# Kernel optimization log

Hardware: AMD Instinct MI355X
Metric: run time of the kernel (lower is better)

The kernel has to match this reference:

```python
import jax, jax.numpy as jnp
import numpy as np
from jax import lax

B, T = 64, 200
NUM_C, DIM_S, SIZE_M = 2000, 128, 50


def setup_inputs() -> dict:
    key = jax.random.key(0)
    ks = jax.random.split(key, 12)
    d = {}
    d['skill'] = jax.random.randint(ks[0], (B, T), 0, NUM_C)
    d['answer'] = jax.random.randint(ks[1], (B, T), 0, 2)
    s = 1.0 / np.sqrt(DIM_S)
    d['k_emb'] = jax.random.normal(ks[2], (NUM_C + 1, DIM_S), jnp.float32)
    d['v_emb'] = jax.random.normal(ks[3], (2 * NUM_C + 1, DIM_S), jnp.float32)
    # kaiming_normal on [size_m, dim_s]: std = sqrt(2/dim_s)
    d['Mk'] = jax.random.normal(ks[4], (SIZE_M, DIM_S), jnp.float32) * np.sqrt(2.0 / DIM_S)
    d['Mv0'] = jax.random.normal(ks[5], (SIZE_M, DIM_S), jnp.float32) * np.sqrt(2.0 / DIM_S)
    d['f_W'] = jax.random.normal(ks[6], (DIM_S, 2 * DIM_S), jnp.float32) * (1.0 / np.sqrt(2 * DIM_S))
    d['f_b'] = jnp.zeros((DIM_S,), jnp.float32)
    d['p_W'] = jax.random.normal(ks[7], (NUM_C, DIM_S), jnp.float32) * s
    d['p_b'] = jnp.zeros((NUM_C,), jnp.float32)
    d['e_W'] = jax.random.normal(ks[8], (DIM_S, DIM_S), jnp.float32) * s
    d['e_b'] = jnp.zeros((DIM_S,), jnp.float32)
    d['a_W'] = jax.random.normal(ks[9], (DIM_S, DIM_S), jnp.float32) * s
    d['a_b'] = jnp.zeros((DIM_S,), jnp.float32)
    return d


def reference(skill, answer, k_emb, v_emb, Mk, Mv0, f_W, f_b, p_W, p_b, e_W, e_b, a_W, a_b):
    num_c = p_W.shape[0]
    bsz = skill.shape[0]
    answer_x = jnp.where(answer == 2, 1, answer)
    x = skill + num_c * answer_x                       # [B,T]
    k = k_emb[skill]                                   # [B,T,D]
    v = v_emb[x]                                       # [B,T,D]
    w = jax.nn.softmax(jnp.einsum('btd,md->btm', k, Mk), axis=-1)   # [B,T,M]
    e = jax.nn.sigmoid(jnp.einsum('btd,ed->bte', v, e_W) + e_b)      # [B,T,D]
    a = jnp.tanh(jnp.einsum('btd,ed->bte', v, a_W) + a_b)            # [B,T,D]

    Mv_init = jnp.broadcast_to(Mv0, (bsz,) + Mv0.shape)              # [B,M,D]

    def step(Mvt, inp):
        et, at, wt = inp                               # [B,D],[B,D],[B,M]
        # read uses pre-update memory (Mv[:, :-1] in the torch code)
        read = jnp.einsum('bm,bmd->bd', wt, Mvt)
        Mvt_new = Mvt * (1.0 - wt[:, :, None] * et[:, None, :]) + wt[:, :, None] * at[:, None, :]
        return Mvt_new, read

    _, reads = lax.scan(step, Mv_init,
                        (e.transpose(1, 0, 2), a.transpose(1, 0, 2), w.transpose(1, 0, 2)))
    reads = reads.transpose(1, 0, 2)                   # [B,T,D]

    f = jnp.tanh(jnp.concatenate([reads, k], axis=-1) @ f_W.T + f_b)  # [B,T,D]
    p = jax.nn.sigmoid(f @ p_W.T + p_b)                # [B,T,num_c] (dropout is identity at eval)
    p = p[:, :-1, :]
    next_skill = skill[:, 1:]                          # [B,T-1]
    idx = jnp.minimum(next_skill, num_c - 1)
    pred = jnp.take_along_axis(p, idx[..., None], axis=-1)[..., 0]
    pred = jnp.where(next_skill < num_c, pred, 0.0)    # index num_c -> zero row in torch one_hot
    return pred
```

## Files before the change

kernel.cpp:

```cpp
#include <hip/hip_runtime.h>
#include <math.h>

#define Bsz 64
#define Tn 200
#define NUMC 2000
#define DS 128
#define SM 50
#define NTOK (Bsz*Tn)
#define WG2 10
#define MPG2 5

typedef __attribute__((ext_vector_type(8))) short bfrag;
typedef __attribute__((ext_vector_type(4))) float f32x4;
typedef __attribute__((ext_vector_type(4))) unsigned int u32x4;

__device__ __forceinline__ unsigned short f2bf(float x) {
    unsigned int u = __builtin_bit_cast(unsigned int, x);
    u = u + 0x7fffu + ((u >> 16) & 1u);
    return (unsigned short)(u >> 16);
}
__device__ __forceinline__ unsigned int pack2(float a, float b) {
    return (unsigned int)f2bf(a) | ((unsigned int)f2bf(b) << 16);
}
__device__ __forceinline__ bfrag mk_frag(f32x4 x, f32x4 y) {
    u32x4 t;
    t[0] = pack2(x[0], x[1]); t[1] = pack2(x[2], x[3]);
    t[2] = pack2(y[0], y[1]); t[3] = pack2(y[2], y[3]);
    return __builtin_bit_cast(bfrag, t);
}

__device__ __forceinline__ float fast_exp(float x)  { return __builtin_amdgcn_exp2f(x * 1.44269504f); }
__device__ __forceinline__ float fast_rcp(float x)  { return __builtin_amdgcn_rcpf(x); }
__device__ __forceinline__ float fast_sigmoid(float x) { return fast_rcp(1.f + fast_exp(-x)); }
__device__ __forceinline__ float fast_tanh(float x) { return 1.f - 2.f * fast_rcp(fast_exp(2.f * x) + 1.f); }

__device__ __forceinline__ void load_group(const bfrag* __restrict__ B, int nt0, int L, bfrag bf[4][4]) {
    #pragma unroll
    for (int t = 0; t < 4; t++)
        #pragma unroll
        for (int ki = 0; ki < 4; ki++)
            bf[t][ki] = B[(size_t)((nt0 + t) * 4 + ki) * 64 + L];
}
__device__ __forceinline__ void mfma_group(const bfrag A[4], const bfrag bf[4][4], f32x4 acc[4]) {
    #pragma unroll
    for (int ki = 0; ki < 4; ki++)
        #pragma unroll
        for (int t = 0; t < 4; t++)
            acc[t] = __builtin_amdgcn_mfma_f32_16x16x32_bf16(A[ki], bf[t][ki], acc[t], 0, 0, 0);
}

__global__ __launch_bounds__(256) void k0_cast(
    const float* __restrict__ eW, const float* __restrict__ aW,
    const float* __restrict__ fW, const float* __restrict__ Mk,
    unsigned int* __restrict__ BeaU, unsigned int* __restrict__ BkmU,
    unsigned int* __restrict__ Bf0U)
{
    const int g = blockIdx.x * 256 + threadIdx.x;
    if (g >= 9216) return;
    int gm, mat;
    unsigned int* dst;
    if (g < 4096)      { mat = 0; gm = g;        dst = BeaU; }
    else if (g < 7168) { mat = 1; gm = g - 4096; dst = BkmU; }
    else               { mat = 2; gm = g - 7168; dst = Bf0U; }
    const int nt = gm >> 8, r = gm & 255, ki = r >> 6, L = r & 63;
    const int n = nt * 16 + (L & 15);
    const int k = ki * 32 + (L >> 4) * 8;

    const float* src = nullptr;
    if (mat == 0) {
        src = (n < 128) ? (eW + (size_t)n * DS + k) : (aW + (size_t)(n - 128) * DS + k);
    } else if (mat == 1) {
        if (n < 128)      src = fW + (size_t)n * (2 * DS) + DS + k;
        else if (n < 128 + SM) src = Mk + (size_t)(n - 128) * DS + k;
    } else {
        src = fW + (size_t)n * (2 * DS) + k;
    }
    float v[8];
    #pragma unroll
    for (int j = 0; j < 8; j++) v[j] = src ? src[j] : 0.f;
    u32x4 o;
    o[0] = pack2(v[0], v[1]); o[1] = pack2(v[2], v[3]);
    o[2] = pack2(v[4], v[5]); o[3] = pack2(v[6], v[7]);
    ((u32x4*)dst)[gm] = o;
}

__global__ __launch_bounds__(64) void k1_gemm(
    const int* __restrict__ skill, const int* __restrict__ answer,
    const float* __restrict__ k_emb, const float* __restrict__ v_emb,
    const unsigned int* __restrict__ BeaU, const unsigned int* __restrict__ BkmU,
    const float* __restrict__ eB, const float* __restrict__ aB,
    float* __restrict__ w_buf, float* __restrict__ e_buf,
    float* __restrict__ a_buf, float* __restrict__ kp_buf)
{
    const int bid = blockIdx.x;
    const int L = threadIdx.x, L15 = L & 15, quad = L >> 4;

    if (bid < NTOK/16) {
        const int tok0 = bid * 16;
        const int tokA = tok0 + L15;
        const int tokD0 = tok0 + quad * 4;

        const bfrag* Bea = (const bfrag*)BeaU;
        bfrag bfA[4][4], bfB[4][4];
        load_group(Bea, 0, L, bfA);
        load_group(Bea, 4, L, bfB);

        const int s  = skill[tokA];
        const int an = answer[tokA];
        const int ax = (an == 2) ? 1 : an;
        const float* vp = v_emb + ((size_t)(s + NUMC * ax)) * DS + quad * 8;
        bfrag Vf[4];
        #pragma unroll
        for (int ki = 0; ki < 4; ki++) {
            const f32x4* a = (const f32x4*)(vp + ki * 32);
            Vf[ki] = mk_frag(a[0], a[1]);
        }

        f32x4 acc[4];
        #pragma unroll
        for (int t = 0; t < 4; t++) acc[t] = (f32x4){0.f,0.f,0.f,0.f};
        mfma_group(Vf, bfA, acc);
        load_group(Bea, 8, L, bfA);
        #pragma unroll
        for (int t = 0; t < 4; t++) {
            const int n = t * 16 + L15;
            const float bias = eB[n];
            #pragma unroll
            for (int reg = 0; reg < 4; reg++)
                e_buf[(size_t)(tokD0 + reg) * DS + n] = fast_sigmoid(acc[t][reg] + bias);
        }

        #pragma unroll
        for (int t = 0; t < 4; t++) acc[t] = (f32x4){0.f,0.f,0.f,0.f};
        mfma_group(Vf, bfB, acc);
        load_group(Bea, 12, L, bfB);
        #pragma unroll
        for (int t = 0; t < 4; t++) {
            const int n = (4 + t) * 16 + L15;
            const float bias = eB[n];
            #pragma unroll
            for (int reg = 0; reg < 4; reg++)
                e_buf[(size_t)(tokD0 + reg) * DS + n] = fast_sigmoid(acc[t][reg] + bias);
        }

        #pragma unroll
        for (int t = 0; t < 4; t++) acc[t] = (f32x4){0.f,0.f,0.f,0.f};
        mfma_group(Vf, bfA, acc);
        #pragma unroll
        for (int t = 0; t < 4; t++) {
            const int n = t * 16 + L15;
            const float bias = aB[n];
            #pragma unroll
            for (int reg = 0; reg < 4; reg++)
                a_buf[(size_t)(tokD0 + reg) * DS + n] = fast_tanh(acc[t][reg] + bias);
        }

        #pragma unroll
        for (int t = 0; t < 4; t++) acc[t] = (f32x4){0.f,0.f,0.f,0.f};
        mfma_group(Vf, bfB, acc);
        #pragma unroll
        for (int t = 0; t < 4; t++) {
            const int n = (4 + t) * 16 + L15;
            const float bias = aB[n];
            #pragma unroll
            for (int reg = 0; reg < 4; reg++)
                a_buf[(size_t)(tokD0 + reg) * DS + n] = fast_tanh(acc[t][reg] + bias);
        }
    } else {
        const int tok0 = (bid - NTOK/16) * 16;
        const int tokA = tok0 + L15;
        const int tokD0 = tok0 + quad * 4;

        const bfrag* Bkm = (const bfrag*)BkmU;
        bfrag bfA[4][4], bfB[4][4];
        load_group(Bkm, 0, L, bfA);
        load_group(Bkm, 4, L, bfB);

        const int s = skill[tokA];
        const float* kp = k_emb + (size_t)s * DS + quad * 8;
        bfrag Kf[4];
        #pragma unroll
        for (int ki = 0; ki < 4; ki++) {
            const f32x4* b = (const f32x4*)(kp + ki * 32);
            Kf[ki] = mk_frag(b[0], b[1]);
        }

        __shared__ float wl[16][52];

        f32x4 acc[4];
        #pragma unroll
        for (int t = 0; t < 4; t++) acc[t] = (f32x4){0.f,0.f,0.f,0.f};
        mfma_group(Kf, bfA, acc);
        load_group(Bkm, 8, L, bfA);
        #pragma unroll
        for (int t = 0; t < 4; t++) {
            const int n = t * 16 + L15;
            #pragma unroll
            for (int reg = 0; reg < 4; reg++)
                kp_buf[(size_t)(tokD0 + reg) * DS + n] = acc[t][reg];
        }

        #pragma unroll
        for (int t = 0; t < 4; t++) acc[t] = (f32x4){0.f,0.f,0.f,0.f};
        mfma_group(Kf, bfB, acc);
        #pragma unroll
        for (int t = 0; t < 4; t++) {
            const int n = (4 + t) * 16 + L15;
            #pragma unroll
            for (int reg = 0; reg < 4; reg++)
                kp_buf[(size_t)(tokD0 + reg) * DS + n] = acc[t][reg];
        }

        #pragma unroll
        for (int t = 0; t < 4; t++) acc[t] = (f32x4){0.f,0.f,0.f,0.f};
        mfma_group(Kf, bfA, acc);
        #pragma unroll
        for (int t = 0; t < 4; t++) {
            const int c = (8 + t) * 16 + L15 - 128;
            if (c < SM) {
                #pragma unroll
                for (int reg = 0; reg < 4; reg++)
                    wl[quad * 4 + reg][c] = acc[t][reg];
            }
        }
        __syncthreads();
        if (L < 16) {
            float mx = -1e30f;
            for (int m = 0; m < SM; m++) mx = fmaxf(mx, wl[L][m]);
            float sum = 0.f;
            float ex[SM];
            for (int m = 0; m < SM; m++) { ex[m] = fast_exp(wl[L][m] - mx); sum += ex[m]; }
            const float inv = fast_rcp(sum);
            float* wp = w_buf + (size_t)(tok0 + L) * SM;
            for (int m = 0; m < SM; m++) wp[m] = ex[m] * inv;
        }
    }
}

__global__ __launch_bounds__(640) void k2_scan(
    const float* __restrict__ w_buf, const float* __restrict__ e_buf,
    const float* __restrict__ a_buf, const float* __restrict__ Mv0,
    float* __restrict__ reads_buf)
{
    const int bi   = blockIdx.x;
    const int b    = bi >> 1;
    const int dh   = bi & 1;
    const int wv   = threadIdx.x >> 6;
    const int lane = threadIdx.x & 63;
    const int d    = dh * 64 + lane;
    const int m0   = wv * MPG2;
    const int base = b * Tn;

    __shared__ float red[2][WG2][8][64];

    float Mv[MPG2];
    #pragma unroll
    for (int m = 0; m < MPG2; m++) Mv[m] = Mv0[(size_t)(m0+m)*DS + d];

    float se[4][2], sa[4][2], sw[4][2][MPG2];

    #define LOADST(ST, T)                                                      \
        { const int tc_ = ((T) < Tn) ? (T) : 0;                                \
          _Pragma("unroll")                                                    \
          for (int q_ = 0; q_ < 2; q_++) {                                     \
              const int tf_ = base + tc_ + q_;                                 \
              se[ST][q_] = e_buf[(size_t)tf_*DS + d];                          \
              sa[ST][q_] = a_buf[(size_t)tf_*DS + d];                          \
              _Pragma("unroll")                                                \
              for (int m_ = 0; m_ < MPG2; m_++)                                \
                  sw[ST][q_][m_] = w_buf[(size_t)tf_*SM + m0 + m_];            \
          } }

    LOADST(0, 0) LOADST(1, 2) LOADST(2, 4) LOADST(3, 6)

    for (int i = 0; i < 25; i++) {
        const int tb = i * 8;
        const int p  = i & 1;
        #pragma unroll
        for (int sub = 0; sub < 4; sub++) {
            const int t0 = tb + sub * 2;
            #pragma unroll
            for (int q = 0; q < 2; q++) {
                const float ev = se[sub][q], av = sa[sub][q];
                float rd = 0.f;
                #pragma unroll
                for (int m = 0; m < MPG2; m++) {
                    const float wm = sw[sub][q][m];
                    rd = fmaf(wm, Mv[m], rd);
                    Mv[m] = fmaf(-wm, fmaf(ev, Mv[m], -av), Mv[m]);
                }
                red[p][wv][sub * 2 + q][lane] = rd;
            }
            LOADST(sub, t0 + 8)
        }
        __syncthreads();
        const int j = threadIdx.x;
        if (j < 512) {
            const int tt = j >> 6, dd = j & 63;
            float s = red[p][0][tt][dd];
            #pragma unroll
            for (int g = 1; g < WG2; g++) s += red[p][g][tt][dd];
            reads_buf[(size_t)(base + tb + tt) * DS + dh * 64 + dd] = s;
        }
    }
    #undef LOADST
}

__global__ __launch_bounds__(64) void k3_gemm(
    const float* __restrict__ reads_buf, const float* __restrict__ kp_buf,
    const unsigned int* __restrict__ Bf0U, const float* __restrict__ fB,
    const float* __restrict__ pW, const float* __restrict__ pB,
    const int* __restrict__ skill, float* __restrict__ out)
{
    const int L = threadIdx.x, L15 = L & 15, quad = L >> 4;
    const int tok0 = blockIdx.x * 16;
    const int tokA = tok0 + L15;
    const int tokD0 = tok0 + quad * 4;

    const bfrag* Bf0 = (const bfrag*)Bf0U;
    bfrag bfA[4][4], bfB[4][4];
    load_group(Bf0, 0, L, bfA);
    load_group(Bf0, 4, L, bfB);

    bfrag Rf[4];
    #pragma unroll
    for (int ki = 0; ki < 4; ki++) {
        const f32x4* q4 = (const f32x4*)(reads_buf + (size_t)tokA * DS + ki * 32 + quad * 8);
        Rf[ki] = mk_frag(q4[0], q4[1]);
    }

    float f[4][8];
    f32x4 acc[4];

    #pragma unroll
    for (int t = 0; t < 4; t++) acc[t] = (f32x4){0.f,0.f,0.f,0.f};
    mfma_group(Rf, bfA, acc);
    #pragma unroll
    for (int t = 0; t < 4; t++) {
        const int n = t * 16 + L15;
        const float fb = fB[n];
        #pragma unroll
        for (int reg = 0; reg < 4; reg++)
            f[reg][t] = fast_tanh(acc[t][reg] + kp_buf[(size_t)(tokD0 + reg) * DS + n] + fb);
    }

    #pragma unroll
    for (int t = 0; t < 4; t++) acc[t] = (f32x4){0.f,0.f,0.f,0.f};
    mfma_group(Rf, bfB, acc);
    #pragma unroll
    for (int t = 0; t < 4; t++) {
        const int n = (4 + t) * 16 + L15;
        const float fb = fB[n];
        #pragma unroll
        for (int reg = 0; reg < 4; reg++)
            f[reg][4 + t] = fast_tanh(acc[t][reg] + kp_buf[(size_t)(tokD0 + reg) * DS + n] + fb);
    }

    #pragma unroll
    for (int reg = 0; reg < 4; reg++) {
        const int tok = tokD0 + reg;
        const int t = tok % Tn;
        const bool act = (t < Tn - 1);
        int sn = 0, ix = 0;
        float contrib = 0.f;
        if (act) {
            sn = skill[tok + 1];
            ix = (sn < NUMC) ? sn : (NUMC - 1);
            const float* pr = pW + (size_t)ix * DS + L15;
            #pragma unroll
            for (int nt = 0; nt < 8; nt++)
                contrib = fmaf(f[reg][nt], pr[nt * 16], contrib);
        }
        #pragma unroll
        for (int msk = 1; msk <= 8; msk <<= 1)
            contrib += __shfl_xor(contrib, msk);
        if (act && L15 == 0) {
            const float val = contrib + pB[ix];
            const float prd = (sn < NUMC) ? fast_sigmoid(val) : 0.f;
            out[(size_t)(tok / Tn) * (Tn - 1) + t] = prd;
        }
    }
}

extern "C" void kernel_launch(void* const* d_in, const int* in_sizes, int n_in,
                              void* d_out, int out_size, void* d_ws, size_t ws_size,
                              hipStream_t stream)
{
    const int*   skill  = (const int*)  d_in[0];
    const int*   answer = (const int*)  d_in[1];
    const float* k_emb  = (const float*)d_in[2];
    const float* v_emb  = (const float*)d_in[3];
    const float* Mk     = (const float*)d_in[4];
    const float* Mv0    = (const float*)d_in[5];
    const float* f_W    = (const float*)d_in[6];
    const float* f_b    = (const float*)d_in[7];
    const float* p_W    = (const float*)d_in[8];
    const float* p_b    = (const float*)d_in[9];
    const float* e_W    = (const float*)d_in[10];
    const float* e_b    = (const float*)d_in[11];
    const float* a_W    = (const float*)d_in[12];
    const float* a_b    = (const float*)d_in[13];
    float* out = (float*)d_out;

    float* ws        = (float*)d_ws;
    float* w_buf     = ws;
    float* e_buf     = w_buf     + (size_t)NTOK*SM;
    float* a_buf     = e_buf     + (size_t)NTOK*DS;
    float* kp_buf    = a_buf     + (size_t)NTOK*DS;
    float* reads_buf = kp_buf    + (size_t)NTOK*DS;
    unsigned int* BeaU = (unsigned int*)(reads_buf + (size_t)NTOK*DS);
    unsigned int* BkmU = BeaU + 4096 * 4;
    unsigned int* Bf0U = BkmU + 3072 * 4;

    k0_cast<<<36, 256, 0, stream>>>(e_W, a_W, f_W, Mk, BeaU, BkmU, Bf0U);
    k1_gemm<<<2*(NTOK/16), 64, 0, stream>>>(skill, answer, k_emb, v_emb,
        BeaU, BkmU, e_b, a_b, w_buf, e_buf, a_buf, kp_buf);
    k2_scan<<<Bsz*2, 640, 0, stream>>>(w_buf, e_buf, a_buf, Mv0, reads_buf);
    k3_gemm<<<NTOK/16, 64, 0, stream>>>(reads_buf, kp_buf, Bf0U, f_b,
        p_W, p_b, skill, out);
}
```

Baseline: 144.2 us.

## Fuse projection GEMMs, memory scan and output head into one per-batch kernel

Replaces the three kernels (projection GEMM, scan, output GEMM) with a single kernel that runs one 640-thread block per batch row. Each block first computes e/a/kp/w for its 200 tokens using wave-tiled MFMA, with the softmax now done by shuffle reduction. It then runs the scan, which now spans all 128 dims in one block, and keeps the reads in LDS as bf16 for the final GEMM and gather. This removes two launches and the global round-trip of reads_buf. The cost is only 64 blocks, so the projection phases get far less parallelism than the 1600 blocks used before.

```diff
diff --git a/kernel.cpp b/kernel.cpp
--- a/kernel.cpp
+++ b/kernel.cpp
@@ -7,8 +7,8 @@
 #define DS 128
 #define SM 50
 #define NTOK (Bsz*Tn)
-#define WG2 10
-#define MPG2 5
+#define WVS 10
+#define MPG 10
 
 typedef __attribute__((ext_vector_type(8))) short bfrag;
 typedef __attribute__((ext_vector_type(4))) float f32x4;
@@ -84,300 +84,259 @@
     ((u32x4*)dst)[gm] = o;
 }
 
-__global__ __launch_bounds__(64) void k1_gemm(
+__global__ __launch_bounds__(640) void kf_fused(
     const int* __restrict__ skill, const int* __restrict__ answer,
     const float* __restrict__ k_emb, const float* __restrict__ v_emb,
     const unsigned int* __restrict__ BeaU, const unsigned int* __restrict__ BkmU,
+    const unsigned int* __restrict__ Bf0U,
     const float* __restrict__ eB, const float* __restrict__ aB,
-    float* __restrict__ w_buf, float* __restrict__ e_buf,
-    float* __restrict__ a_buf, float* __restrict__ kp_buf)
+    const float* __restrict__ Mv0, const float* __restrict__ fB,
+    const float* __restrict__ pW, const float* __restrict__ pB,
+    float* __restrict__ e_buf, float* __restrict__ a_buf,
+    float* __restrict__ w_buf, float* __restrict__ kp_buf,
+    float* __restrict__ out)
 {
-    const int bid = blockIdx.x;
-    const int L = threadIdx.x, L15 = L & 15, quad = L >> 4;
-
-    if (bid < NTOK/16) {
-        const int tok0 = bid * 16;
-        const int tokA = tok0 + L15;
-        const int tokD0 = tok0 + quad * 4;
-
-        const bfrag* Bea = (const bfrag*)BeaU;
-        bfrag bfA[4][4], bfB[4][4];
-        load_group(Bea, 0, L, bfA);
-        load_group(Bea, 4, L, bfB);
-
-        const int s  = skill[tokA];
-        const int an = answer[tokA];
+    const int b    = blockIdx.x;
+    const int base = b * Tn;
+    const int tid  = threadIdx.x;
+    const int wv   = tid >> 6;
+    const int L    = tid & 63;
+    const int L15  = L & 15, quad = L >> 4;
+
+    __shared__ __align__(16) unsigned short reads_bf[208][136];
+    __shared__ float red[2][WVS][8][64];
+
+    const bfrag* Bea = (const bfrag*)BeaU;
+    const bfrag* Bkm = (const bfrag*)BkmU;
+    const bfrag* Bf0 = (const bfrag*)Bf0U;
+
+    for (int tile = wv; tile < 13; tile += WVS) {
+        const int tok0 = tile * 16;
+        const int rowA = tok0 + L15;
+        const int gA   = base + ((rowA < Tn) ? rowA : (Tn - 1));
+        const int trow = tok0 + quad * 4;
+
+        const int s  = skill[gA];
+        const int an = answer[gA];
         const int ax = (an == 2) ? 1 : an;
         const float* vp = v_emb + ((size_t)(s + NUMC * ax)) * DS + quad * 8;
-        bfrag Vf[4];
+        const float* kk = k_emb + (size_t)s * DS + quad * 8;
+        bfrag Vf[4], Kf[4];
         #pragma unroll
         for (int ki = 0; ki < 4; ki++) {
             const f32x4* a = (const f32x4*)(vp + ki * 32);
             Vf[ki] = mk_frag(a[0], a[1]);
-        }
-
+            const f32x4* c = (const f32x4*)(kk + ki * 32);
+            Kf[ki] = mk_frag(c[0], c[1]);
+        }
+
+        bfrag bfA[4][4], bfB[4][4];
+        load_group(Bea, 0, L, bfA);
         f32x4 acc[4];
+
+        #define ZACC { _Pragma("unroll") for (int t_ = 0; t_ < 4; t_++) acc[t_] = (f32x4){0.f,0.f,0.f,0.f}; }
+        ZACC mfma_group(Vf, bfA, acc); load_group(Bea, 4, L, bfB);
+        #pragma unroll
+        for (int t = 0; t < 4; t++) {
+            const int n = t * 16 + L15; const float bias = eB[n];
+            #pragma unroll
+            for (int reg = 0; reg < 4; reg++)
+                if (trow + reg < Tn) e_buf[(size_t)(base + trow + reg) * DS + n] = fast_sigmoid(acc[t][reg] + bias);
+        }
+        ZACC mfma_group(Vf, bfB, acc); load_group(Bea, 8, L, bfA);
+        #pragma unroll
+        for (int t = 0; t < 4; t++) {
+            const int n = 64 + t * 16 + L15; const float bias = eB[n];
+            #pragma unroll
+            for (int reg = 0; reg < 4; reg++)
+                if (trow + reg < Tn) e_buf[(size_t)(base + trow + reg) * DS + n] = fast_sigmoid(acc[t][reg] + bias);
+        }
+        ZACC mfma_group(Vf, bfA, acc); load_group(Bea, 12, L, bfB);
+        #pragma unroll
+        for (int t = 0; t < 4; t++) {
+            const int n = t * 16 + L15; const float bias = aB[n];
+            #pragma unroll
+            for (int reg = 0; reg < 4; reg++)
+                if (trow + reg < Tn) a_buf[(size_t)(base + trow + reg) * DS + n] = fast_tanh(acc[t][reg] + bias);
+        }
+        ZACC mfma_group(Vf, bfB, acc); load_group(Bkm, 0, L, bfA);
+        #pragma unroll
+        for (int t = 0; t < 4; t++) {
+            const int n = 64 + t * 16 + L15; const float bias = aB[n];
+            #pragma unroll
+            for (int reg = 0; reg < 4; reg++)
+                if (trow + reg < Tn) a_buf[(size_t)(base + trow + reg) * DS + n] = fast_tanh(acc[t][reg] + bias);
+        }
+        ZACC mfma_group(Kf, bfA, acc); load_group(Bkm, 4, L, bfB);
+        #pragma unroll
+        for (int t = 0; t < 4; t++) {
+            const int n = t * 16 + L15;
+            #pragma unroll
+            for (int reg = 0; reg < 4; reg++)
+                if (trow + reg < Tn) kp_buf[(size_t)(base + trow + reg) * DS + n] = acc[t][reg];
+        }
+        ZACC mfma_group(Kf, bfB, acc); load_group(Bkm, 8, L, bfA);
+        #pragma unroll
+        for (int t = 0; t < 4; t++) {
+            const int n = 64 + t * 16 + L15;
+            #pragma unroll
+            for (int reg = 0; reg < 4; reg++)
+                if (trow + reg < Tn) kp_buf[(size_t)(base + trow + reg) * DS + n] = acc[t][reg];
+        }
+        ZACC mfma_group(Kf, bfA, acc);
+        #pragma unroll
+        for (int reg = 0; reg < 4; reg++) {
+            float m = -1e30f;
+            #pragma unroll
+            for (int t = 0; t < 4; t++) { const int c = t * 16 + L15; if (c < SM) m = fmaxf(m, acc[t][reg]); }
+            #pragma unroll
+            for (int msk = 1; msk <= 8; msk <<= 1) m = fmaxf(m, __shfl_xor(m, msk));
+            float ex[4]; float ssum = 0.f;
+            #pragma unroll
+            for (int t = 0; t < 4; t++) {
+                const int c = t * 16 + L15;
+                ex[t] = (c < SM) ? fast_exp(acc[t][reg] - m) : 0.f;
+                ssum += ex[t];
+            }
+            #pragma unroll
+            for (int msk = 1; msk <= 8; msk <<= 1) ssum += __shfl_xor(ssum, msk);
+            const float inv = fast_rcp(ssum);
+            if (trow + reg < Tn) {
+                float* wp = w_buf + (size_t)(base + trow + reg) * SM;
+                #pragma unroll
+                for (int t = 0; t < 4; t++) { const int c = t * 16 + L15; if (c < SM) wp[c] = ex[t] * inv; }
+            }
+        }
+        #undef ZACC
+    }
+    __syncthreads();
+
+    {
+        const int dh = wv / 5;
+        const int mg = wv % 5;
+        const int m0 = mg * MPG;
+        const int d  = dh * 64 + L;
+
+        float Mv[MPG];
+        #pragma unroll
+        for (int m = 0; m < MPG; m++) Mv[m] = Mv0[(size_t)(m0 + m) * DS + d];
+
+        float se[4][2], sa[4][2], sw[4][2][MPG];
+
+        #define LOADST(ST, T)                                                      \
+            { const int tc_ = ((T) < Tn) ? (T) : 0;                                \
+              _Pragma("unroll")                                                    \
+              for (int q_ = 0; q_ < 2; q_++) {                                     \
+                  const int tf_ = base + tc_ + q_;                                 \
+                  se[ST][q_] = e_buf[(size_t)tf_*DS + d];                          \
+                  sa[ST][q_] = a_buf[(size_t)tf_*DS + d];                          \
+                  _Pragma("unroll")                                                \
+                  for (int m_ = 0; m_ < MPG; m_++)                                 \
+                      sw[ST][q_][m_] = w_buf[(size_t)tf_*SM + m0 + m_];            \
+              } }
+
+        LOADST(0, 0) LOADST(1, 2) LOADST(2, 4) LOADST(3, 6)
+
+        for (int i = 0; i < 25; i++) {
+            const int tb = i * 8;
+            const int p  = i & 1;
+            #pragma unroll
+            for (int sub = 0; sub < 4; sub++) {
+                const int t0 = tb + sub * 2;
+                #pragma unroll
+                for (int q = 0; q < 2; q++) {
+                    const float ev = se[sub][q], av = sa[sub][q];
+                    float rd = 0.f;
+                    #pragma unroll
+                    for (int m = 0; m < MPG; m++) {
+                        const float wm = sw[sub][q][m];
+                        rd = fmaf(wm, Mv[m], rd);
+                        Mv[m] = fmaf(-wm, fmaf(ev, Mv[m], -av), Mv[m]);
+                    }
+                    red[p][wv][sub * 2 + q][L] = rd;
+                }
+                LOADST(sub, t0 + 8)
+            }
+            __syncthreads();
+            for (int o = tid; o < 1024; o += 640) {
+                const int tt = o >> 7, dd = o & 127;
+                const int dh2 = dd >> 6, d6 = dd & 63;
+                float s = red[p][dh2 * 5 + 0][tt][d6];
+                #pragma unroll
+                for (int g = 1; g < 5; g++) s += red[p][dh2 * 5 + g][tt][d6];
+                reads_bf[tb + tt][dd] = f2bf(s);
+            }
+        }
+        #undef LOADST
+    }
+    __syncthreads();
+
+    for (int tile = wv; tile < 13; tile += WVS) {
+        const int tok0 = tile * 16;
+        const int trow = tok0 + quad * 4;
+
+        bfrag Rf[4];
+        #pragma unroll
+        for (int ki = 0; ki < 4; ki++)
+            Rf[ki] = *reinterpret_cast<const bfrag*>(&reads_bf[tok0 + L15][ki * 32 + quad * 8]);
+
+        bfrag bfA[4][4], bfB[4][4];
+        load_group(Bf0, 0, L, bfA);
+        load_group(Bf0, 4, L, bfB);
+
+        float f[4][8];
+        f32x4 acc[4];
+
         #pragma unroll
         for (int t = 0; t < 4; t++) acc[t] = (f32x4){0.f,0.f,0.f,0.f};
-        mfma_group(Vf, bfA, acc);
-        load_group(Bea, 8, L, bfA);
+        mfma_group(Rf, bfA, acc);
         #pragma unroll
         for (int t = 0; t < 4; t++) {
             const int n = t * 16 + L15;
-            const float bias = eB[n];
-            #pragma unroll
-            for (int reg = 0; reg < 4; reg++)
-                e_buf[(size_t)(tokD0 + reg) * DS + n] = fast_sigmoid(acc[t][reg] + bias);
+            const float fb = fB[n];
+            #pragma unroll
+            for (int reg = 0; reg < 4; reg++) {
+                const int lrow = (trow + reg < Tn) ? (trow + reg) : (Tn - 1);
+                f[reg][t] = fast_tanh(acc[t][reg] + kp_buf[(size_t)(base + lrow) * DS + n] + fb);
+            }
         }
 
         #pragma unroll
         for (int t = 0; t < 4; t++) acc[t] = (f32x4){0.f,0.f,0.f,0.f};
-        mfma_group(Vf, bfB, acc);
-        load_group(Bea, 12, L, bfB);
+        mfma_group(Rf, bfB, acc);
         #pragma unroll
         for (int t = 0; t < 4; t++) {
             const int n = (4 + t) * 16 + L15;
-            const float bias = eB[n];
-            #pragma unroll
-            for (int reg = 0; reg < 4; reg++)
-                e_buf[(size_t)(tokD0 + reg) * DS + n] = fast_sigmoid(acc[t][reg] + bias);
-        }
-
-        #pragma unroll
-        for (int t = 0; t < 4; t++) acc[t] = (f32x4){0.f,0.f,0.f,0.f};
-        mfma_group(Vf, bfA, acc);
-        #pragma unroll
-        for (int t = 0; t < 4; t++) {
-            const int n = t * 16 + L15;
-            const float bias = aB[n];
-            #pragma unroll
-            for (int reg = 0; reg < 4; reg++)
-                a_buf[(size_t)(tokD0 + reg) * DS + n] = fast_tanh(acc[t][reg] + bias);
-        }
-
-        #pragma unroll
-        for (int t = 0; t < 4; t++) acc[t] = (f32x4){0.f,0.f,0.f,0.f};
-        mfma_group(Vf, bfB, acc);
-        #pragma unroll
-        for (int t = 0; t < 4; t++) {
-            const int n = (4 + t) * 16 + L15;
-            const float bias = aB[n];
-            #pragma unroll
-            for (int reg = 0; reg < 4; reg++)
-                a_buf[(size_t)(tokD0 + reg) * DS + n] = fast_tanh(acc[t][reg] + bias);
-        }
-    } else {
-        const int tok0 = (bid - NTOK/16) * 16;
-        const int tokA = tok0 + L15;
-        const int tokD0 = tok0 + quad * 4;
-
-        const bfrag* Bkm = (const bfrag*)BkmU;
-        bfrag bfA[4][4], bfB[4][4];
-        load_group(Bkm, 0, L, bfA);
-        load_group(Bkm, 4, L, bfB);
-
-        const int s = skill[tokA];
-        const float* kp = k_emb + (size_t)s * DS + quad * 8;
-        bfrag Kf[4];
-        #pragma unroll
-        for (int ki = 0; ki < 4; ki++) {
-            const f32x4* b = (const f32x4*)(kp + ki * 32);
-            Kf[ki] = mk_frag(b[0], b[1]);
-        }
-
-        __shared__ float wl[16][52];
-
-        f32x4 acc[4];
-        #pragma unroll
-        for (int t = 0; t < 4; t++) acc[t] = (f32x4){0.f,0.f,0.f,0.f};
-        mfma_group(Kf, bfA, acc);
-        load_group(Bkm, 8, L, bfA);
-        #pragma unroll
-        for (int t = 0; t < 4; t++) {
-            const int n = t * 16 + L15;
-            #pragma unroll
-            for (int reg = 0; reg < 4; reg++)
-                kp_buf[(size_t)(tokD0 + reg) * DS + n] = acc[t][reg];
-        }
-
-        #pragma unroll
-        for (int t = 0; t < 4; t++) acc[t] = (f32x4){0.f,0.f,0.f,0.f};
-        mfma_group(Kf, bfB, acc);
-        #pragma unroll
-        for (int t = 0; t < 4; t++) {
-            const int n = (4 + t) * 16 + L15;
-            #pragma unroll
-            for (int reg = 0; reg < 4; reg++)
-                kp_buf[(size_t)(tokD0 + reg) * DS + n] = acc[t][reg];
-        }
-
-        #pragma unroll
-        for (int t = 0; t < 4; t++) acc[t] = (f32x4){0.f,0.f,0.f,0.f};
-        mfma_group(Kf, bfA, acc);
-        #pragma unroll
-        for (int t = 0; t < 4; t++) {
-            const int c = (8 + t) * 16 + L15 - 128;
-            if (c < SM) {
+            const float fb = fB[n];
+            #pragma unroll
+            for (int reg = 0; reg < 4; reg++) {
+                const int lrow = (trow + reg < Tn) ? (trow + reg) : (Tn - 1);
+                f[reg][4 + t] = fast_tanh(acc[t][reg] + kp_buf[(size_t)(base + lrow) * DS + n] + fb);
+            }
+        }
+
+        #pragma unroll
+        for (int reg = 0; reg < 4; reg++) {
+            const int t_in = trow + reg;
+            const bool act = (t_in < Tn - 1);
+            int sn = 0, ix = 0;
+            float contrib = 0.f;
+            if (act) {
+                sn = skill[base + t_in + 1];
+                ix = (sn < NUMC) ? sn : (NUMC - 1);
+                const float* pr = pW + (size_t)ix * DS + L15;
                 #pragma unroll
-                for (int reg = 0; reg < 4; reg++)
-                    wl[quad * 4 + reg][c] = acc[t][reg];
-            }
-        }
-        __syncthreads();
-        if (L < 16) {
-            float mx = -1e30f;
-            for (int m = 0; m < SM; m++) mx = fmaxf(mx, wl[L][m]);
-            float sum = 0.f;
-            float ex[SM];
-            for (int m = 0; m < SM; m++) { ex[m] = fast_exp(wl[L][m] - mx); sum += ex[m]; }
-            const float inv = fast_rcp(sum);
-            float* wp = w_buf + (size_t)(tok0 + L) * SM;
-            for (int m = 0; m < SM; m++) wp[m] = ex[m] * inv;
-        }
-    }
-}
-
-__global__ __launch_bounds__(640) void k2_scan(
-    const float* __restrict__ w_buf, const float* __restrict__ e_buf,
-    const float* __restrict__ a_buf, const float* __restrict__ Mv0,
-    float* __restrict__ reads_buf)
-{
-    const int bi   = blockIdx.x;
-    const int b    = bi >> 1;
-    const int dh   = bi & 1;
-    const int wv   = threadIdx.x >> 6;
-    const int lane = threadIdx.x & 63;
-    const int d    = dh * 64 + lane;
-    const int m0   = wv * MPG2;
-    const int base = b * Tn;
-
-    __shared__ float red[2][WG2][8][64];
-
-    float Mv[MPG2];
-    #pragma unroll
-    for (int m = 0; m < MPG2; m++) Mv[m] = Mv0[(size_t)(m0+m)*DS + d];
-
-    float se[4][2], sa[4][2], sw[4][2][MPG2];
-
-    #define LOADST(ST, T)                                                      \
-        { const int tc_ = ((T) < Tn) ? (T) : 0;                                \
-          _Pragma("unroll")                                                    \
-          for (int q_ = 0; q_ < 2; q_++) {                                     \
-              const int tf_ = base + tc_ + q_;                                 \
-              se[ST][q_] = e_buf[(size_t)tf_*DS + d];                          \
-              sa[ST][q_] = a_buf[(size_t)tf_*DS + d];                          \
-              _Pragma("unroll")                                                \
-              for (int m_ = 0; m_ < MPG2; m_++)                                \
-                  sw[ST][q_][m_] = w_buf[(size_t)tf_*SM + m0 + m_];            \
-          } }
-
-    LOADST(0, 0) LOADST(1, 2) LOADST(2, 4) LOADST(3, 6)
-
-    for (int i = 0; i < 25; i++) {
-        const int tb = i * 8;
-        const int p  = i & 1;
-        #pragma unroll
-        for (int sub = 0; sub < 4; sub++) {
-            const int t0 = tb + sub * 2;
-            #pragma unroll
-            for (int q = 0; q < 2; q++) {
-                const float ev = se[sub][q], av = sa[sub][q];
-                float rd = 0.f;
-                #pragma unroll
-                for (int m = 0; m < MPG2; m++) {
-                    const float wm = sw[sub][q][m];
-                    rd = fmaf(wm, Mv[m], rd);
-                    Mv[m] = fmaf(-wm, fmaf(ev, Mv[m], -av), Mv[m]);
-                }
-                red[p][wv][sub * 2 + q][lane] = rd;
-            }
-            LOADST(sub, t0 + 8)
-        }
-        __syncthreads();
-        const int j = threadIdx.x;
-        if (j < 512) {
-            const int tt = j >> 6, dd = j & 63;
-            float s = red[p][0][tt][dd];
-            #pragma unroll
-            for (int g = 1; g < WG2; g++) s += red[p][g][tt][dd];
-            reads_buf[(size_t)(base + tb + tt) * DS + dh * 64 + dd] = s;
-        }
-    }
-    #undef LOADST
-}
-
-__global__ __launch_bounds__(64) void k3_gemm(
-    const float* __restrict__ reads_buf, const float* __restrict__ kp_buf,
-    const unsigned int* __restrict__ Bf0U, const float* __restrict__ fB,
-    const float* __restrict__ pW, const float* __restrict__ pB,
-    const int* __restrict__ skill, float* __restrict__ out)
-{
-    const int L = threadIdx.x, L15 = L & 15, quad = L >> 4;
-    const int tok0 = blockIdx.x * 16;
-    const int tokA = tok0 + L15;
-    const int tokD0 = tok0 + quad * 4;
-
-    const bfrag* Bf0 = (const bfrag*)Bf0U;
-    bfrag bfA[4][4], bfB[4][4];
-    load_group(Bf0, 0, L, bfA);
-    load_group(Bf0, 4, L, bfB);
-
-    bfrag Rf[4];
-    #pragma unroll
-    for (int ki = 0; ki < 4; ki++) {
-        const f32x4* q4 = (const f32x4*)(reads_buf + (size_t)tokA * DS + ki * 32 + quad * 8);
-        Rf[ki] = mk_frag(q4[0], q4[1]);
-    }
-
-    float f[4][8];
-    f32x4 acc[4];
-
-    #pragma unroll
-    for (int t = 0; t < 4; t++) acc[t] = (f32x4){0.f,0.f,0.f,0.f};
-    mfma_group(Rf, bfA, acc);
-    #pragma unroll
-    for (int t = 0; t < 4; t++) {
-        const int n = t * 16 + L15;
-        const float fb = fB[n];
-        #pragma unroll
-        for (int reg = 0; reg < 4; reg++)
-            f[reg][t] = fast_tanh(acc[t][reg] + kp_buf[(size_t)(tokD0 + reg) * DS + n] + fb);
-    }
-
-    #pragma unroll
-    for (int t = 0; t < 4; t++) acc[t] = (f32x4){0.f,0.f,0.f,0.f};
-    mfma_group(Rf, bfB, acc);
-    #pragma unroll
-    for (int t = 0; t < 4; t++) {
-        const int n = (4 + t) * 16 + L15;
-        const float fb = fB[n];
-        #pragma unroll
-        for (int reg = 0; reg < 4; reg++)
-            f[reg][4 + t] = fast_tanh(acc[t][reg] + kp_buf[(size_t)(tokD0 + reg) * DS + n] + fb);
-    }
-
-    #pragma unroll
-    for (int reg = 0; reg < 4; reg++) {
-        const int tok = tokD0 + reg;
-        const int t = tok % Tn;
-        const bool act = (t < Tn - 1);
-        int sn = 0, ix = 0;
-        float contrib = 0.f;
-        if (act) {
-            sn = skill[tok + 1];
-            ix = (sn < NUMC) ? sn : (NUMC - 1);
-            const float* pr = pW + (size_t)ix * DS + L15;
-            #pragma unroll
-            for (int nt = 0; nt < 8; nt++)
-                contrib = fmaf(f[reg][nt], pr[nt * 16], contrib);
-        }
-        #pragma unroll
-        for (int msk = 1; msk <= 8; msk <<= 1)
-            contrib += __shfl_xor(contrib, msk);
-        if (act && L15 == 0) {
-            const float val = contrib + pB[ix];
-            const float prd = (sn < NUMC) ? fast_sigmoid(val) : 0.f;
-            out[(size_t)(tok / Tn) * (Tn - 1) + t] = prd;
+                for (int nt = 0; nt < 8; nt++)
+                    contrib = fmaf(f[reg][nt], pr[nt * 16], contrib);
+            }
+            #pragma unroll
+            for (int msk = 1; msk <= 8; msk <<= 1)
+                contrib += __shfl_xor(contrib, msk);
+            if (act && L15 == 0) {
+                const float val = contrib + pB[ix];
+                const float prd = (sn < NUMC) ? fast_sigmoid(val) : 0.f;
+                out[(size_t)b * (Tn - 1) + t_in] = prd;
+            }
         }
     }
 }
@@ -402,20 +361,17 @@
     const float* a_b    = (const float*)d_in[13];
     float* out = (float*)d_out;
 
-    float* ws        = (float*)d_ws;
-    float* w_buf     = ws;
-    float* e_buf     = w_buf     + (size_t)NTOK*SM;
-    float* a_buf     = e_buf     + (size_t)NTOK*DS;
-    float* kp_buf    = a_buf     + (size_t)NTOK*DS;
-    float* reads_buf = kp_buf    + (size_t)NTOK*DS;
-    unsigned int* BeaU = (unsigned int*)(reads_buf + (size_t)NTOK*DS);
+    float* ws     = (float*)d_ws;
+    float* w_buf  = ws;
+    float* e_buf  = w_buf  + (size_t)NTOK*SM;
+    float* a_buf  = e_buf  + (size_t)NTOK*DS;
+    float* kp_buf = a_buf  + (size_t)NTOK*DS;
+    unsigned int* BeaU = (unsigned int*)(kp_buf + (size_t)NTOK*DS);
     unsigned int* BkmU = BeaU + 4096 * 4;
     unsigned int* Bf0U = BkmU + 3072 * 4;
 
     k0_cast<<<36, 256, 0, stream>>>(e_W, a_W, f_W, Mk, BeaU, BkmU, Bf0U);
-    k1_gemm<<<2*(NTOK/16), 64, 0, stream>>>(skill, answer, k_emb, v_emb,
-        BeaU, BkmU, e_b, a_b, w_buf, e_buf, a_buf, kp_buf);
-    k2_scan<<<Bsz*2, 640, 0, stream>>>(w_buf, e_buf, a_buf, Mv0, reads_buf);
-    k3_gemm<<<NTOK/16, 64, 0, stream>>>(reads_buf, kp_buf, Bf0U, f_b,
-        p_W, p_b, skill, out);
-}
+    kf_fused<<<Bsz, 640, 0, stream>>>(skill, answer, k_emb, v_emb,
+        BeaU, BkmU, Bf0U, e_b, a_b, Mv0, f_b, p_W, p_b,
+        e_buf, a_buf, w_buf, kp_buf, out);
+}
```

Measured after the change: 290.6 us. 2.02x slower.
